# Kernel tuning notes

Hardware: AMD Instinct MI355X
Metric: run time of the kernel (lower is better)

Reference implementation:

```python
import jax, jax.numpy as jnp
import numpy as np

B, N, T, D = 8, 32, 32, 4      # batch, num_atoms, time_steps, dims
K, H, P = 2, 256, 4            # edge_types, decoder_hidden, pred_steps
E = N * (N - 1)                # num directed edges, no self loop
TAU = 0.5                      # gumbel-softmax temperature (hard=False, dropout p=0)


def _onehot_edges():
    idx = np.array([(r, s) for r in range(N) for s in range(N) if r != s], dtype=np.int64)
    eye = np.eye(N, dtype=np.float32)
    return jnp.asarray(eye[idx[:, 0]]), jnp.asarray(eye[idx[:, 1]])  # rel_rec, rel_send [E,N]


def setup_inputs() -> dict:
    key = jax.random.key(0)
    ks = jax.random.split(key, 10)
    rel_rec, rel_send = _onehot_edges()
    u = jax.random.uniform(ks[1], (1, 1, E, K), jnp.float32, 1e-10, 1.0)
    s = 0.05
    return {
        'inputs': jax.random.normal(ks[0], (B, N, T, D), jnp.float32),
        'rel_graph': jax.random.normal(ks[2], (1, 1, E, K), jnp.float32) * (2.0 / (E + K)) ** 0.5,
        'W1': jax.random.normal(ks[3], (K, 2 * D, H), jnp.float32) * s,
        'b1': jnp.zeros((K, H), jnp.float32),
        'W2': jax.random.normal(ks[4], (K, H, H), jnp.float32) * s,
        'b2': jnp.zeros((K, H), jnp.float32),
        'Wo1': jax.random.normal(ks[5], (D + H, H), jnp.float32) * s,
        'bo1': jnp.zeros((H,), jnp.float32),
        'Wo2': jax.random.normal(ks[6], (H, H), jnp.float32) * s,
        'bo2': jnp.zeros((H,), jnp.float32),
        'Wo3': jax.random.normal(ks[7], (H, D), jnp.float32) * s,
        'bo3': jnp.zeros((D,), jnp.float32),
        'rel_rec': rel_rec,
        'rel_send': rel_send,
        'gumbel': -jnp.log(-jnp.log(u)),
    }


def reference(inputs, rel_graph, W1, b1, W2, b2, Wo1, bo1, Wo2, bo2, Wo3, bo3, rel_rec, rel_send, gumbel):
    # gumbel_softmax(rel_graph, tau, hard=False) with fixed gumbel noise
    edges = jax.nn.softmax((rel_graph + gumbel) / TAU, axis=-1)   # [1,1,E,K]
    x = inputs.transpose(0, 2, 1, 3)                              # [B,T,N,D]
    last = x[:, 0::P]                                             # [B,Tp,N,D], Tp = T//P
    preds, hooks = [], []
    for _ in range(P):
        recv = jnp.einsum('en,btnd->bted', rel_rec, last)         # gather receivers
        send = jnp.einsum('en,btnd->bted', rel_send, last)        # gather senders
        pre_msg = jnp.concatenate([send, recv], axis=-1)          # [B,Tp,E,2D]
        all_msgs = jnp.zeros(pre_msg.shape[:3] + (H,), pre_msg.dtype)
        m = None
        for i in range(K):                                        # skip_first=False -> all edge types
            m = jax.nn.relu(pre_msg @ W1[i] + b1[i])              # dropout p=0 -> identity
            m = jax.nn.relu(m @ W2[i] + b2[i])
            m = m * edges[..., i:i + 1]
            all_msgs = all_msgs + m
        hooks.append(m.transpose(1, 0, 2, 3))                     # msg_hook: last type's msg, [Tp,B,E,H]
        agg = jnp.einsum('bteh,en->btnh', all_msgs, rel_rec)      # scatter-sum messages to receivers
        aug = jnp.concatenate([last, agg], axis=-1)               # [B,Tp,N,D+H]
        p = jax.nn.relu(aug @ Wo1 + bo1)
        p = jax.nn.relu(p @ Wo2 + bo2)
        p = p @ Wo3 + bo3
        last = last + p                                           # residual update
        preds.append(last)
    # interleave: output[:, i::P] = preds[i]  ->  time index j*P + i
    out = jnp.stack(preds, axis=2).reshape(B, -1, N, D)           # [B,Tp*P,N,D]
    pred_all = out[:, :T - 1].transpose(0, 2, 1, 3)               # [B,N,T-1,D]
    rel_out = jnp.broadcast_to(rel_graph[:, 0], (B, E, K))
    return pred_all, rel_out, jnp.concatenate(hooks, axis=0)
```

## Files before the change

kernel.cpp:

```cpp
#include <hip/hip_runtime.h>

typedef unsigned short u16;
typedef unsigned int   u32;
typedef unsigned long long u64;
typedef __attribute__((ext_vector_type(8))) short bf16x8;
typedef __attribute__((ext_vector_type(4))) float f32x4;

__device__ __forceinline__ float bf2f(u16 s){ u32 u = ((u32)s)<<16; float f; __builtin_memcpy(&f,&u,4); return f; }
__device__ __forceinline__ u16 f2bf(float f){
  u32 u; __builtin_memcpy(&u,&f,4);
  u32 r = u + 0x7fffu + ((u>>16)&1u);
  return (u16)(r>>16);
}
__device__ __forceinline__ float inV(const void* p, int i, int F){
  return F ? bf2f(((const u16*)p)[i]) : ((const float*)p)[i];
}

__device__ __forceinline__ void detect_bf16(const void* inputs0, int tid, int* flagL){
  if (tid < 64){
    const uint4* dp = (const uint4*)inputs0;
    uint4 v = dp[tid];
    u32 wds[4] = {v.x, v.y, v.z, v.w};
    int sus = 0;
#pragma unroll
    for (int i2=0; i2<4; ++i2){
      u32 wv = wds[i2];
      u32 h0 = wv & 0xffffu, h1 = wv >> 16;
      if (((h0>>7)&0xffu) >= 0xA0u) sus = 1;
      if (((h1>>7)&0xffu) >= 0xA0u) sus = 1;
    }
    u64 bal = __ballot(sus);
    if (tid == 0) *flagL = (bal == 0ull) ? 1 : 0;
  }
}

#define WS_LAST0 0
#define WS_LAST1 32768
#define WS_WF    65536
#define WS_W2P   720896
#define WS_AGG   1245184

#define WF_W1   0
#define WF_B1   4096
#define WF_B2   4608
#define WF_WO1  5120
#define WF_BO1  71680
#define WF_WO2  71936
#define WF_BO2  137472
#define WF_WO3  137728
#define WF_BO3  138752
#define WF_EV   138756

#define PR_WF   138756
#define PR_EV   (PR_WF + 992)
#define PR_L0   (PR_EV + 8192)
#define PR_RO   (PR_L0 + 15872)
#define PR_W2P  (PR_RO + 262144)

__global__ void k_prep(const void* __restrict__ inputs, const void* __restrict__ rel_graph,
                       const void* __restrict__ gumbel,
                       const void* __restrict__ W1, const void* __restrict__ b1,
                       const void* __restrict__ W2, const void* __restrict__ b2,
                       const void* __restrict__ Wo1, const void* __restrict__ bo1,
                       const void* __restrict__ Wo2, const void* __restrict__ bo2,
                       const void* __restrict__ Wo3, const void* __restrict__ bo3,
                       float* __restrict__ wf, u16* __restrict__ w2p,
                       float* __restrict__ last0, float* __restrict__ out)
{
  __shared__ int flagL;
  int tid = threadIdx.x;
  detect_bf16(inputs, tid, &flagL);
  __syncthreads();
  const int F = flagL;
  int i = blockIdx.x*256 + tid;
  if (i < PR_WF){
    const void* src; int off;
    if      (i < 4096)   { src = W1;  off = i; }
    else if (i < 4608)   { src = b1;  off = i-4096; }
    else if (i < 5120)   { src = b2;  off = i-4608; }
    else if (i < 71680)  { src = Wo1; off = i-5120; }
    else if (i < 71936)  { src = bo1; off = i-71680; }
    else if (i < 137472) { src = Wo2; off = i-71936; }
    else if (i < 137728) { src = bo2; off = i-137472; }
    else if (i < 138752) { src = Wo3; off = i-137728; }
    else                 { src = bo3; off = i-138752; }
    wf[i] = inV(src, off, F);
    return;
  }
  if (i < PR_EV){
    int e = i - PR_WF;
    float l0 = (inV(rel_graph,2*e,F)   + inV(gumbel,2*e,F))   * 2.f;
    float l1 = (inV(rel_graph,2*e+1,F) + inV(gumbel,2*e+1,F)) * 2.f;
    float m = fmaxf(l0,l1);
    float e0 = __expf(l0-m), e1 = __expf(l1-m), s = 1.f/(e0+e1);
    wf[WF_EV+2*e]   = e0*s;
    wf[WF_EV+2*e+1] = e1*s;
    return;
  }
  if (i < PR_L0){
    int j = i - PR_EV;
    int d = j&3, n = (j>>2)&31, bt = j>>7, b = bt>>3, tp = bt&7;
    last0[j] = inV(inputs, b*4096 + n*128 + tp*16 + d, F);
    return;
  }
  if (i < PR_RO){
    int j = i - PR_L0;
    out[31744 + j] = inV(rel_graph, j % 1984, F);
    return;
  }
  if (i < PR_W2P){
    int e = i - PR_RO;
    int ei = e & 7, l = (e>>3)&63, q = (e>>9)&7, t = (e>>12)&15,
        part = (e>>16)&1, k = e>>17;
    int kk  = q*32 + (l>>4)*8 + ei;
    int col = t*16 + (l&15);
    float f = inV(W2, k*65536 + kk*256 + col, F);
    u16 h = f2bf(f);
    w2p[e] = part ? f2bf(f - bf2f(h)) : h;
  }
}

__device__ __forceinline__ void fma4(float4& a, float s, float4 w){
  a.x += s*w.x; a.y += s*w.y; a.z += s*w.z; a.w += s*w.w;
}

__global__ __launch_bounds__(256) void k_msg(
    const float* __restrict__ lastIn, const float* __restrict__ wf,
    const u16* __restrict__ w2p, float* __restrict__ agg,
    float* __restrict__ hooks, int pstep)
{
  __shared__ float xj[32][8];
  __shared__ float evL[31][2];
  __shared__ uint4 AhF[16][64];
  __shared__ uint4 AlF[16][64];

  const int tid = threadIdx.x;
  const int n = blockIdx.x & 31, bt = blockIdx.x >> 5;
  const int b = bt>>3, tp = bt&7;
  const int rg = tid & 7, cgi = tid >> 3, c = cgi*8;
  const int lane = tid & 63, wave = tid >> 6;
  const int l15 = lane & 15, lg = lane >> 4;

  if (tid < 32){
    int j = tid;
    float4 sv = make_float4(0.f,0.f,0.f,0.f), rv = sv;
    if (j < 31){
      int s = j + (j >= n);
      sv = *(const float4*)&lastIn[bt*128 + s*4];
      rv = *(const float4*)&lastIn[bt*128 + n*4];
    }
    *(float4*)&xj[j][0] = sv;
    *(float4*)&xj[j][4] = rv;
  } else if (tid < 63){
    int j = tid - 32, e = n*31 + j;
    evL[j][0] = wf[WF_EV + 2*e];
    evL[j][1] = wf[WF_EV + 2*e + 1];
  }
  __syncthreads();

  const int hb = (((pstep*8 + tp)*8 + b)*992 + n*31)*256;
  float aggl[4] = {0.f,0.f,0.f,0.f};

  for (int k=0; k<2; ++k){
    float4 a0[4], a1[4];
    {
      float4 bb0 = *(const float4*)&wf[WF_B1 + k*256 + c];
      float4 bb1 = *(const float4*)&wf[WF_B1 + k*256 + c + 4];
#pragma unroll
      for (int ri=0; ri<4; ++ri){ a0[ri] = bb0; a1[ri] = bb1; }
      const float* W1k = wf + WF_W1 + k*2048;
#pragma unroll
      for (int kd=0; kd<8; ++kd){
        float4 w0 = *(const float4*)&W1k[kd*256 + c];
        float4 w1 = *(const float4*)&W1k[kd*256 + c + 4];
#pragma unroll
        for (int ri=0; ri<4; ++ri){
          float xv = xj[rg + 8*ri][kd];
          fma4(a0[ri], xv, w0); fma4(a1[ri], xv, w1);
        }
      }
    }
    if (k) __syncthreads();
#pragma unroll
    for (int ri=0; ri<4; ++ri){
      int j = rg + 8*ri;
      float v[8] = { fmaxf(a0[ri].x,0.f), fmaxf(a0[ri].y,0.f),
                     fmaxf(a0[ri].z,0.f), fmaxf(a0[ri].w,0.f),
                     fmaxf(a1[ri].x,0.f), fmaxf(a1[ri].y,0.f),
                     fmaxf(a1[ri].z,0.f), fmaxf(a1[ri].w,0.f) };
      u32 hw[4], lw[4];
#pragma unroll
      for (int e2=0; e2<4; ++e2){
        u16 h0 = f2bf(v[2*e2]),   h1 = f2bf(v[2*e2+1]);
        u16 g0 = f2bf(v[2*e2]   - bf2f(h0));
        u16 g1 = f2bf(v[2*e2+1] - bf2f(h1));
        hw[e2] = (u32)h0 | ((u32)h1<<16);
        lw[e2] = (u32)g0 | ((u32)g1<<16);
      }
      int fi   = ((j>>4)<<3) + (cgi>>2);
      int slot = (j&15) + ((cgi&3)<<4);
      AhF[fi][slot] = make_uint4(hw[0],hw[1],hw[2],hw[3]);
      AlF[fi][slot] = make_uint4(lw[0],lw[1],lw[2],lw[3]);
    }
    __syncthreads();

    f32x4 acc[2][4];
#pragma unroll
    for (int nt=0; nt<4; ++nt){
      float bv = wf[WF_B2 + k*256 + wave*64 + nt*16 + l15];
      f32x4 t = {bv,bv,bv,bv};
      acc[0][nt] = t; acc[1][nt] = t;
    }
    const u16* W2pk = w2p + k*131072;
#pragma unroll 2
    for (int q=0; q<8; ++q){
      bf16x8 Ah0 = __builtin_bit_cast(bf16x8, AhF[q][lane]);
      bf16x8 Ah1 = __builtin_bit_cast(bf16x8, AhF[8+q][lane]);
      bf16x8 Al0 = __builtin_bit_cast(bf16x8, AlF[q][lane]);
      bf16x8 Al1 = __builtin_bit_cast(bf16x8, AlF[8+q][lane]);
#pragma unroll
      for (int nt=0; nt<4; ++nt){
        int tt = wave*4 + nt;
        const u16* bp = W2pk + ((tt*8 + q)*64 + lane)*8;
        bf16x8 Bh = __builtin_bit_cast(bf16x8, *(const uint4*)bp);
        bf16x8 Bl = __builtin_bit_cast(bf16x8, *(const uint4*)(bp + 65536));
        acc[0][nt] = __builtin_amdgcn_mfma_f32_16x16x32_bf16(Ah0, Bh, acc[0][nt], 0,0,0);
        acc[1][nt] = __builtin_amdgcn_mfma_f32_16x16x32_bf16(Ah1, Bh, acc[1][nt], 0,0,0);
        acc[0][nt] = __builtin_amdgcn_mfma_f32_16x16x32_bf16(Al0, Bh, acc[0][nt], 0,0,0);
        acc[1][nt] = __builtin_amdgcn_mfma_f32_16x16x32_bf16(Al1, Bh, acc[1][nt], 0,0,0);
        acc[0][nt] = __builtin_amdgcn_mfma_f32_16x16x32_bf16(Ah0, Bl, acc[0][nt], 0,0,0);
        acc[1][nt] = __builtin_amdgcn_mfma_f32_16x16x32_bf16(Ah1, Bl, acc[1][nt], 0,0,0);
      }
    }

#pragma unroll
    for (int rt=0; rt<2; ++rt){
#pragma unroll
      for (int r=0; r<4; ++r){
        int j = rt*16 + lg*4 + r;
        if (j < 31){
          float ev = evL[j][k];
#pragma unroll
          for (int nt=0; nt<4; ++nt){
            float m = fmaxf(acc[rt][nt][r], 0.f) * ev;
            aggl[nt] += m;
            if (k == 1) hooks[hb + j*256 + wave*64 + nt*16 + l15] = m;
          }
        }
      }
    }
  }

#pragma unroll
  for (int nt=0; nt<4; ++nt){
    aggl[nt] += __shfl_xor(aggl[nt], 16);
    aggl[nt] += __shfl_xor(aggl[nt], 32);
  }
  if (lane < 16){
#pragma unroll
    for (int nt=0; nt<4; ++nt)
      agg[blockIdx.x*256 + wave*64 + nt*16 + lane] = aggl[nt];
  }
}

__global__ __launch_bounds__(256) void k_out(
    const float* __restrict__ lastIn, float* __restrict__ lastOut,
    const float* __restrict__ wf, const float* __restrict__ agg,
    float* __restrict__ out0, int pstep)
{
  __shared__ float augT[8][264];
  __shared__ float o1T[8][264];
  __shared__ float o2T[8][264];
  const int tid = threadIdx.x;
  const int r0 = blockIdx.x*8;

#pragma unroll
  for (int rr=0; rr<8; ++rr) augT[rr][4+tid] = agg[(r0+rr)*256 + tid];
  if (tid < 32){
    int rr = tid>>2, d = tid&3, r = r0+rr;
    augT[rr][d] = lastIn[(r>>5)*128 + (r&31)*4 + d];
  }
  __syncthreads();
  {
    float acc[8];
    float bv = wf[WF_BO1 + tid];
#pragma unroll
    for (int rr=0; rr<8; ++rr) acc[rr] = bv;
    for (int i4=0; i4<260; i4+=4){
      float w0 = wf[WF_WO1 + (i4+0)*256 + tid];
      float w1 = wf[WF_WO1 + (i4+1)*256 + tid];
      float w2 = wf[WF_WO1 + (i4+2)*256 + tid];
      float w3 = wf[WF_WO1 + (i4+3)*256 + tid];
#pragma unroll
      for (int rr=0; rr<8; ++rr){
        float4 x = *(const float4*)&augT[rr][i4];
        acc[rr] += x.x*w0 + x.y*w1 + x.z*w2 + x.w*w3;
      }
    }
#pragma unroll
    for (int rr=0; rr<8; ++rr) o1T[rr][tid] = fmaxf(acc[rr], 0.f);
  }
  __syncthreads();
  {
    float acc[8];
    float bv = wf[WF_BO2 + tid];
#pragma unroll
    for (int rr=0; rr<8; ++rr) acc[rr] = bv;
    for (int i4=0; i4<256; i4+=4){
      float w0 = wf[WF_WO2 + (i4+0)*256 + tid];
      float w1 = wf[WF_WO2 + (i4+1)*256 + tid];
      float w2 = wf[WF_WO2 + (i4+2)*256 + tid];
      float w3 = wf[WF_WO2 + (i4+3)*256 + tid];
#pragma unroll
      for (int rr=0; rr<8; ++rr){
        float4 x = *(const float4*)&o1T[rr][i4];
        acc[rr] += x.x*w0 + x.y*w1 + x.z*w2 + x.w*w3;
      }
    }
#pragma unroll
    for (int rr=0; rr<8; ++rr) o2T[rr][tid] = fmaxf(acc[rr], 0.f);
  }
  __syncthreads();
  if (tid < 64){
    int d = tid&3, half = (tid>>2)&1, r = tid>>3;
    float p = 0.f;
    for (int ii=0; ii<128; ++ii){
      int i = half*128 + ii;
      p += o2T[r][i]*wf[WF_WO3 + i*4 + d];
    }
    p += __shfl_xor(p, 4);
    if (!half){
      int row = r0 + r, bt = row>>5, nn = row&31;
      float lv = lastIn[bt*128 + nn*4 + d] + p + wf[WF_BO3 + d];
      lastOut[bt*128 + nn*4 + d] = lv;
      int bb = bt>>3, tp = bt&7, t = tp*4 + pstep;
      if (t < 31) out0[bb*3968 + nn*124 + t*4 + d] = lv;
    }
  }
}

extern "C" void kernel_launch(void* const* d_in, const int* in_sizes, int n_in,
                              void* d_out, int out_size, void* d_ws, size_t ws_size,
                              hipStream_t stream) {
  const void* inputs    = d_in[0];
  const void* rel_graph = d_in[1];
  const void* W1  = d_in[2];
  const void* b1  = d_in[3];
  const void* W2  = d_in[4];
  const void* b2  = d_in[5];
  const void* Wo1 = d_in[6];
  const void* bo1 = d_in[7];
  const void* Wo2 = d_in[8];
  const void* bo2 = d_in[9];
  const void* Wo3 = d_in[10];
  const void* bo3 = d_in[11];
  const void* gumbel = d_in[14];
  float* out = (float*)d_out;
  char* ws = (char*)d_ws;
  float* L0   = (float*)(ws + WS_LAST0);
  float* L1   = (float*)(ws + WS_LAST1);
  float* wf   = (float*)(ws + WS_WF);
  u16*   w2p  = (u16*)  (ws + WS_W2P);
  float* aggp = (float*)(ws + WS_AGG);

  k_prep<<<(PR_W2P + 255)/256, 256, 0, stream>>>(
      inputs, rel_graph, gumbel, W1, b1, W2, b2, Wo1, bo1, Wo2, bo2, Wo3, bo3,
      wf, w2p, L0, out);
  for (int p = 0; p < 4; ++p) {
    const float* lin  = (p & 1) ? L1 : L0;
    float*       lout = (p & 1) ? L0 : L1;
    k_msg<<<2048, 256, 0, stream>>>(lin, wf, w2p, aggp, out + 47616, p);
    k_out<<<256, 256, 0, stream>>>(lin, lout, wf, aggp, out, p);
  }
}
```

Measured before the change: 664.4 us.

## Fuse message and output MLP kernels, switch split-bf16 MFMA to single fp16

Merges the per-step message kernel and the node-output MLP kernel into one kernel, so each block handles two batch-time slices for one receiver node and the aggregated messages stay in shared memory instead of a global round trip. The W2 GEMM goes from a three-pass split-bf16 scheme to one fp16 MFMA pass. Wo1 and Wo2 are pre-transposed and stored as fp16 for vectorized loads. Hook writes are staged through shared memory for coalesced float4 stores. The costs are lower precision in W2 and the output weights, with possible fp16 overflow or accuracy loss, and fewer blocks per launch.

```diff
diff --git a/kernel.cpp b/kernel.cpp
--- a/kernel.cpp
+++ b/kernel.cpp
@@ -3,15 +3,11 @@
 typedef unsigned short u16;
 typedef unsigned int   u32;
 typedef unsigned long long u64;
-typedef __attribute__((ext_vector_type(8))) short bf16x8;
+typedef __attribute__((ext_vector_type(8))) _Float16 f16x8;
 typedef __attribute__((ext_vector_type(4))) float f32x4;
 
 __device__ __forceinline__ float bf2f(u16 s){ u32 u = ((u32)s)<<16; float f; __builtin_memcpy(&f,&u,4); return f; }
-__device__ __forceinline__ u16 f2bf(float f){
-  u32 u; __builtin_memcpy(&u,&f,4);
-  u32 r = u + 0x7fffu + ((u>>16)&1u);
-  return (u16)(r>>16);
-}
+__device__ __forceinline__ u16 f2h(float f){ _Float16 h = (_Float16)f; return __builtin_bit_cast(u16, h); }
 __device__ __forceinline__ float inV(const void* p, int i, int F){
   return F ? bf2f(((const u16*)p)[i]) : ((const float*)p)[i];
 }
@@ -37,25 +33,26 @@
 #define WS_LAST0 0
 #define WS_LAST1 32768
 #define WS_WF    65536
-#define WS_W2P   720896
-#define WS_AGG   1245184
+#define WS_W2P   102400
+#define WS_WO1T  364544
+#define WS_WO2T  499712
 
 #define WF_W1   0
 #define WF_B1   4096
 #define WF_B2   4608
-#define WF_WO1  5120
-#define WF_BO1  71680
-#define WF_WO2  71936
-#define WF_BO2  137472
-#define WF_WO3  137728
-#define WF_BO3  138752
-#define WF_EV   138756
-
-#define PR_WF   138756
-#define PR_EV   (PR_WF + 992)
+#define WF_WO3  5120
+#define WF_BO1  6144
+#define WF_BO2  6400
+#define WF_BO3  6656
+#define WF_EV   6664
+
+#define PR_MISC 6660
+#define PR_EV   (PR_MISC + 992)
 #define PR_L0   (PR_EV + 8192)
 #define PR_RO   (PR_L0 + 15872)
-#define PR_W2P  (PR_RO + 262144)
+#define PR_W2P  (PR_RO + 131072)
+#define PR_WO1T (PR_W2P + 67584)
+#define PR_WO2T (PR_WO1T + 65536)
 
 __global__ void k_prep(const void* __restrict__ inputs, const void* __restrict__ rel_graph,
                        const void* __restrict__ gumbel,
@@ -65,6 +62,7 @@
                        const void* __restrict__ Wo2, const void* __restrict__ bo2,
                        const void* __restrict__ Wo3, const void* __restrict__ bo3,
                        float* __restrict__ wf, u16* __restrict__ w2p,
+                       u16* __restrict__ wo1t, u16* __restrict__ wo2t,
                        float* __restrict__ last0, float* __restrict__ out)
 {
   __shared__ int flagL;
@@ -73,22 +71,20 @@
   __syncthreads();
   const int F = flagL;
   int i = blockIdx.x*256 + tid;
-  if (i < PR_WF){
+  if (i < PR_MISC){
     const void* src; int off;
-    if      (i < 4096)   { src = W1;  off = i; }
-    else if (i < 4608)   { src = b1;  off = i-4096; }
-    else if (i < 5120)   { src = b2;  off = i-4608; }
-    else if (i < 71680)  { src = Wo1; off = i-5120; }
-    else if (i < 71936)  { src = bo1; off = i-71680; }
-    else if (i < 137472) { src = Wo2; off = i-71936; }
-    else if (i < 137728) { src = bo2; off = i-137472; }
-    else if (i < 138752) { src = Wo3; off = i-137728; }
-    else                 { src = bo3; off = i-138752; }
+    if      (i < 4096) { src = W1;  off = i; }
+    else if (i < 4608) { src = b1;  off = i-4096; }
+    else if (i < 5120) { src = b2;  off = i-4608; }
+    else if (i < 6144) { src = Wo3; off = i-5120; }
+    else if (i < 6400) { src = bo1; off = i-6144; }
+    else if (i < 6656) { src = bo2; off = i-6400; }
+    else               { src = bo3; off = i-6656; }
     wf[i] = inV(src, off, F);
     return;
   }
   if (i < PR_EV){
-    int e = i - PR_WF;
+    int e = i - PR_MISC;
     float l0 = (inV(rel_graph,2*e,F)   + inV(gumbel,2*e,F))   * 2.f;
     float l1 = (inV(rel_graph,2*e+1,F) + inV(gumbel,2*e+1,F)) * 2.f;
     float m = fmaxf(l0,l1);
@@ -99,8 +95,8 @@
   }
   if (i < PR_L0){
     int j = i - PR_EV;
-    int d = j&3, n = (j>>2)&31, bt = j>>7, b = bt>>3, tp = bt&7;
-    last0[j] = inV(inputs, b*4096 + n*128 + tp*16 + d, F);
+    int d = j&3, nn = (j>>2)&31, bt = j>>7, b = bt>>3, tp = bt&7;
+    last0[j] = inV(inputs, b*4096 + nn*128 + tp*16 + d, F);
     return;
   }
   if (i < PR_RO){
@@ -110,231 +106,271 @@
   }
   if (i < PR_W2P){
     int e = i - PR_RO;
-    int ei = e & 7, l = (e>>3)&63, q = (e>>9)&7, t = (e>>12)&15,
-        part = (e>>16)&1, k = e>>17;
+    int ei = e & 7, l = (e>>3)&63, q = (e>>9)&7, t = (e>>12)&15, k = e>>16;
     int kk  = q*32 + (l>>4)*8 + ei;
     int col = t*16 + (l&15);
-    float f = inV(W2, k*65536 + kk*256 + col, F);
-    u16 h = f2bf(f);
-    w2p[e] = part ? f2bf(f - bf2f(h)) : h;
+    w2p[e] = f2h(inV(W2, k*65536 + kk*256 + col, F));
+    return;
+  }
+  if (i < PR_WO1T){
+    int e = i - PR_W2P;
+    int c = e / 264, ii = e - c*264;
+    wo1t[e] = (ii < 260) ? f2h(inV(Wo1, ii*256 + c, F)) : (u16)0;
+    return;
+  }
+  if (i < PR_WO2T){
+    int e = i - PR_WO1T;
+    int c = e >> 8, ii = e & 255;
+    wo2t[e] = f2h(inV(Wo2, ii*256 + c, F));
   }
 }
 
 __device__ __forceinline__ void fma4(float4& a, float s, float4 w){
   a.x += s*w.x; a.y += s*w.y; a.z += s*w.z; a.w += s*w.w;
 }
-
-__global__ __launch_bounds__(256) void k_msg(
-    const float* __restrict__ lastIn, const float* __restrict__ wf,
-    const u16* __restrict__ w2p, float* __restrict__ agg,
-    float* __restrict__ hooks, int pstep)
+__device__ __forceinline__ float f4e(const float4& v, int e){
+  switch(e){ case 0: return v.x; case 1: return v.y; case 2: return v.z; default: return v.w; }
+}
+
+__global__ __launch_bounds__(256, 4) void k_fused(
+    const float* __restrict__ lastIn, float* __restrict__ lastOut,
+    const float* __restrict__ wf, const u16* __restrict__ w2p,
+    const u16* __restrict__ wo1t, const u16* __restrict__ wo2t,
+    float* __restrict__ hooks, float* __restrict__ out0, int pstep)
 {
-  __shared__ float xj[32][8];
-  __shared__ float evL[31][2];
-  __shared__ uint4 AhF[16][64];
-  __shared__ uint4 AlF[16][64];
+  __shared__ __align__(16) char smemRaw[35584];
+  float (*xj)[8]  = (float(*)[8])smemRaw;
+  float (*evL)[2] = (float(*)[2])(smemRaw + 2048);
+  uint4* AhF   = (uint4*)(smemRaw + 2304);
+  float* hookT = (float*)(smemRaw + 2304);
+  float* augT  = (float*)(smemRaw + 2304);
+  float* o1T   = (float*)(smemRaw + 2304 + 2112);
+  float* o2T   = (float*)(smemRaw + 2304 + 4224);
 
   const int tid = threadIdx.x;
-  const int n = blockIdx.x & 31, bt = blockIdx.x >> 5;
-  const int b = bt>>3, tp = bt&7;
+  const int n = blockIdx.x & 31, btp = blockIdx.x >> 5;
   const int rg = tid & 7, cgi = tid >> 3, c = cgi*8;
   const int lane = tid & 63, wave = tid >> 6;
   const int l15 = lane & 15, lg = lane >> 4;
 
-  if (tid < 32){
-    int j = tid;
+  if (tid < 64){
+    int e = tid & 31, h = tid >> 5, bt = btp*2 + h;
     float4 sv = make_float4(0.f,0.f,0.f,0.f), rv = sv;
-    if (j < 31){
-      int s = j + (j >= n);
+    if (e < 31){
+      int s = e + (e >= n);
       sv = *(const float4*)&lastIn[bt*128 + s*4];
       rv = *(const float4*)&lastIn[bt*128 + n*4];
     }
-    *(float4*)&xj[j][0] = sv;
-    *(float4*)&xj[j][4] = rv;
-  } else if (tid < 63){
-    int j = tid - 32, e = n*31 + j;
-    evL[j][0] = wf[WF_EV + 2*e];
-    evL[j][1] = wf[WF_EV + 2*e + 1];
+    *(float4*)&xj[tid][0] = sv;
+    *(float4*)&xj[tid][4] = rv;
+  } else if (tid < 95){
+    int e = tid - 64;
+    evL[e][0] = wf[WF_EV + 2*(n*31+e)];
+    evL[e][1] = wf[WF_EV + 2*(n*31+e) + 1];
   }
   __syncthreads();
 
-  const int hb = (((pstep*8 + tp)*8 + b)*992 + n*31)*256;
-  float aggl[4] = {0.f,0.f,0.f,0.f};
+  float agg2[2][4] = {{0.f,0.f,0.f,0.f},{0.f,0.f,0.f,0.f}};
 
   for (int k=0; k<2; ++k){
-    float4 a0[4], a1[4];
+    float4 a[8][2];
     {
       float4 bb0 = *(const float4*)&wf[WF_B1 + k*256 + c];
       float4 bb1 = *(const float4*)&wf[WF_B1 + k*256 + c + 4];
 #pragma unroll
-      for (int ri=0; ri<4; ++ri){ a0[ri] = bb0; a1[ri] = bb1; }
+      for (int ri=0; ri<8; ++ri){ a[ri][0] = bb0; a[ri][1] = bb1; }
       const float* W1k = wf + WF_W1 + k*2048;
 #pragma unroll
-      for (int kd=0; kd<8; ++kd){
-        float4 w0 = *(const float4*)&W1k[kd*256 + c];
-        float4 w1 = *(const float4*)&W1k[kd*256 + c + 4];
+      for (int hf=0; hf<2; ++hf){
+        float4 xr[4][2];
 #pragma unroll
         for (int ri=0; ri<4; ++ri){
-          float xv = xj[rg + 8*ri][kd];
-          fma4(a0[ri], xv, w0); fma4(a1[ri], xv, w1);
+          int j = rg + 8*(hf*4+ri);
+          xr[ri][0] = *(const float4*)&xj[j][0];
+          xr[ri][1] = *(const float4*)&xj[j][4];
         }
-      }
-    }
-    if (k) __syncthreads();
-#pragma unroll
-    for (int ri=0; ri<4; ++ri){
-      int j = rg + 8*ri;
-      float v[8] = { fmaxf(a0[ri].x,0.f), fmaxf(a0[ri].y,0.f),
-                     fmaxf(a0[ri].z,0.f), fmaxf(a0[ri].w,0.f),
-                     fmaxf(a1[ri].x,0.f), fmaxf(a1[ri].y,0.f),
-                     fmaxf(a1[ri].z,0.f), fmaxf(a1[ri].w,0.f) };
-      u32 hw[4], lw[4];
-#pragma unroll
-      for (int e2=0; e2<4; ++e2){
-        u16 h0 = f2bf(v[2*e2]),   h1 = f2bf(v[2*e2+1]);
-        u16 g0 = f2bf(v[2*e2]   - bf2f(h0));
-        u16 g1 = f2bf(v[2*e2+1] - bf2f(h1));
-        hw[e2] = (u32)h0 | ((u32)h1<<16);
-        lw[e2] = (u32)g0 | ((u32)g1<<16);
-      }
-      int fi   = ((j>>4)<<3) + (cgi>>2);
-      int slot = (j&15) + ((cgi&3)<<4);
-      AhF[fi][slot] = make_uint4(hw[0],hw[1],hw[2],hw[3]);
-      AlF[fi][slot] = make_uint4(lw[0],lw[1],lw[2],lw[3]);
-    }
-    __syncthreads();
-
-    f32x4 acc[2][4];
-#pragma unroll
-    for (int nt=0; nt<4; ++nt){
-      float bv = wf[WF_B2 + k*256 + wave*64 + nt*16 + l15];
-      f32x4 t = {bv,bv,bv,bv};
-      acc[0][nt] = t; acc[1][nt] = t;
-    }
-    const u16* W2pk = w2p + k*131072;
-#pragma unroll 2
-    for (int q=0; q<8; ++q){
-      bf16x8 Ah0 = __builtin_bit_cast(bf16x8, AhF[q][lane]);
-      bf16x8 Ah1 = __builtin_bit_cast(bf16x8, AhF[8+q][lane]);
-      bf16x8 Al0 = __builtin_bit_cast(bf16x8, AlF[q][lane]);
-      bf16x8 Al1 = __builtin_bit_cast(bf16x8, AlF[8+q][lane]);
-#pragma unroll
-      for (int nt=0; nt<4; ++nt){
-        int tt = wave*4 + nt;
-        const u16* bp = W2pk + ((tt*8 + q)*64 + lane)*8;
-        bf16x8 Bh = __builtin_bit_cast(bf16x8, *(const uint4*)bp);
-        bf16x8 Bl = __builtin_bit_cast(bf16x8, *(const uint4*)(bp + 65536));
-        acc[0][nt] = __builtin_amdgcn_mfma_f32_16x16x32_bf16(Ah0, Bh, acc[0][nt], 0,0,0);
-        acc[1][nt] = __builtin_amdgcn_mfma_f32_16x16x32_bf16(Ah1, Bh, acc[1][nt], 0,0,0);
-        acc[0][nt] = __builtin_amdgcn_mfma_f32_16x16x32_bf16(Al0, Bh, acc[0][nt], 0,0,0);
-        acc[1][nt] = __builtin_amdgcn_mfma_f32_16x16x32_bf16(Al1, Bh, acc[1][nt], 0,0,0);
-        acc[0][nt] = __builtin_amdgcn_mfma_f32_16x16x32_bf16(Ah0, Bl, acc[0][nt], 0,0,0);
-        acc[1][nt] = __builtin_amdgcn_mfma_f32_16x16x32_bf16(Ah1, Bl, acc[1][nt], 0,0,0);
-      }
-    }
-
-#pragma unroll
-    for (int rt=0; rt<2; ++rt){
-#pragma unroll
-      for (int r=0; r<4; ++r){
-        int j = rt*16 + lg*4 + r;
-        if (j < 31){
-          float ev = evL[j][k];
-#pragma unroll
-          for (int nt=0; nt<4; ++nt){
-            float m = fmaxf(acc[rt][nt][r], 0.f) * ev;
-            aggl[nt] += m;
-            if (k == 1) hooks[hb + j*256 + wave*64 + nt*16 + l15] = m;
+#pragma unroll
+        for (int kd=0; kd<8; ++kd){
+          float4 w0 = *(const float4*)&W1k[kd*256 + c];
+          float4 w1 = *(const float4*)&W1k[kd*256 + c + 4];
+#pragma unroll
+          for (int ri=0; ri<4; ++ri){
+            float xv = f4e(xr[ri][kd>>2], kd&3);
+            fma4(a[hf*4+ri][0], xv, w0); fma4(a[hf*4+ri][1], xv, w1);
           }
         }
       }
     }
-  }
-
-#pragma unroll
-  for (int nt=0; nt<4; ++nt){
-    aggl[nt] += __shfl_xor(aggl[nt], 16);
-    aggl[nt] += __shfl_xor(aggl[nt], 32);
-  }
-  if (lane < 16){
-#pragma unroll
-    for (int nt=0; nt<4; ++nt)
-      agg[blockIdx.x*256 + wave*64 + nt*16 + lane] = aggl[nt];
-  }
-}
-
-__global__ __launch_bounds__(256) void k_out(
-    const float* __restrict__ lastIn, float* __restrict__ lastOut,
-    const float* __restrict__ wf, const float* __restrict__ agg,
-    float* __restrict__ out0, int pstep)
-{
-  __shared__ float augT[8][264];
-  __shared__ float o1T[8][264];
-  __shared__ float o2T[8][264];
-  const int tid = threadIdx.x;
-  const int r0 = blockIdx.x*8;
-
-#pragma unroll
-  for (int rr=0; rr<8; ++rr) augT[rr][4+tid] = agg[(r0+rr)*256 + tid];
-  if (tid < 32){
-    int rr = tid>>2, d = tid&3, r = r0+rr;
-    augT[rr][d] = lastIn[(r>>5)*128 + (r&31)*4 + d];
+    if (k) __syncthreads();
+#pragma unroll
+    for (int ri=0; ri<8; ++ri){
+      int j = rg + 8*ri;
+      f16x8 hv;
+#pragma unroll
+      for (int e2=0; e2<8; ++e2)
+        hv[e2] = (_Float16)fmaxf(f4e(a[ri][e2>>2], e2&3), 0.f);
+      int fi   = ((j>>4)<<3) + (cgi>>2);
+      int slot = (j&15) + ((cgi&3)<<4);
+      AhF[fi*64 + slot] = __builtin_bit_cast(uint4, hv);
+    }
+    __syncthreads();
+
+    f32x4 acc[4][4];
+#pragma unroll
+    for (int nt=0; nt<4; ++nt){
+      float bv = wf[WF_B2 + k*256 + (wave<<6) + (nt<<4) + l15];
+      f32x4 bi = {bv,bv,bv,bv};
+#pragma unroll
+      for (int rt=0; rt<4; ++rt) acc[rt][nt] = bi;
+    }
+    const u16* Bbase = w2p + ((k*16 + (wave<<2))*8)*512 + (lane<<3);
+#pragma unroll
+    for (int q=0; q<8; ++q){
+      uint4 Au[4];
+#pragma unroll
+      for (int rt=0; rt<4; ++rt) Au[rt] = AhF[(rt*8+q)*64 + lane];
+#pragma unroll
+      for (int nt=0; nt<4; ++nt){
+        f16x8 Bf = __builtin_bit_cast(f16x8, *(const uint4*)(Bbase + nt*4096 + q*512));
+#pragma unroll
+        for (int rt=0; rt<4; ++rt)
+          acc[rt][nt] = __builtin_amdgcn_mfma_f32_16x16x32_f16(
+              __builtin_bit_cast(f16x8, Au[rt]), Bf, acc[rt][nt], 0,0,0);
+      }
+    }
+
+    if (k == 0){
+#pragma unroll
+      for (int rt=0; rt<4; ++rt){
+#pragma unroll
+        for (int r=0; r<4; ++r){
+          int lr = ((rt&1)<<4) + (lg<<2) + r;
+          if (lr < 31){
+            float ev = evL[lr][0];
+#pragma unroll
+            for (int nt=0; nt<4; ++nt)
+              agg2[rt>>1][nt] += fmaxf(acc[rt][nt][r], 0.f)*ev;
+          }
+        }
+      }
+    } else {
+      __syncthreads();
+#pragma unroll
+      for (int h=0; h<2; ++h){
+#pragma unroll
+        for (int rt2=0; rt2<2; ++rt2){
+          int rt = h*2 + rt2;
+#pragma unroll
+          for (int r=0; r<4; ++r){
+            int lr = (rt2<<4) + (lg<<2) + r;
+            if (lr < 31){
+              float ev = evL[lr][1];
+#pragma unroll
+              for (int nt=0; nt<4; ++nt){
+                float m = fmaxf(acc[rt][nt][r], 0.f)*ev;
+                agg2[h][nt] += m;
+                hookT[lr*260 + (wave<<6) + (nt<<4) + l15] = m;
+              }
+            }
+          }
+        }
+        __syncthreads();
+        {
+          int bt = btp*2 + h, bb = bt>>3, tp = bt&7;
+          int hbh = (((pstep*8 + tp)*8 + bb)*992 + n*31)*256;
+#pragma unroll
+          for (int it=0; it<8; ++it){
+            int row = wave + (it<<2);
+            if (row < 31){
+              float4 v = *(const float4*)&hookT[row*260 + (lane<<2)];
+              *(float4*)&hooks[hbh + row*256 + (lane<<2)] = v;
+            }
+          }
+        }
+        __syncthreads();
+      }
+    }
+  }
+
+#pragma unroll
+  for (int h=0; h<2; ++h)
+#pragma unroll
+    for (int nt=0; nt<4; ++nt){
+      float v = agg2[h][nt];
+      v += __shfl_xor(v, 16);
+      v += __shfl_xor(v, 32);
+      agg2[h][nt] = v;
+    }
+  if (lg == 0){
+#pragma unroll
+    for (int h=0; h<2; ++h)
+#pragma unroll
+      for (int nt=0; nt<4; ++nt)
+        augT[h*264 + 4 + (wave<<6) + (nt<<4) + l15] = agg2[h][nt];
+  }
+  if (tid < 8){
+    int h = tid>>2, d = tid&3;
+    augT[h*264 + d] = lastIn[(btp*2+h)*128 + n*4 + d];
+  } else if (tid < 16){
+    int h = (tid-8)>>2, d = (tid-8)&3;
+    augT[h*264 + 260 + d] = 0.f;
+  }
+  __syncthreads();
+
+  {
+    const u16* wc = wo1t + tid*264;
+    float s0 = wf[WF_BO1 + tid], s1 = s0;
+    for (int i=0; i<264; i+=8){
+      f16x8 hw = __builtin_bit_cast(f16x8, *(const uint4*)(wc + i));
+      float4 xa0 = *(const float4*)&augT[i];
+      float4 xa1 = *(const float4*)&augT[i+4];
+      float4 xb0 = *(const float4*)&augT[264+i];
+      float4 xb1 = *(const float4*)&augT[264+i+4];
+      float w0=(float)hw[0], w1=(float)hw[1], w2=(float)hw[2], w3=(float)hw[3];
+      float w4=(float)hw[4], w5=(float)hw[5], w6=(float)hw[6], w7=(float)hw[7];
+      s0 += xa0.x*w0 + xa0.y*w1 + xa0.z*w2 + xa0.w*w3
+          + xa1.x*w4 + xa1.y*w5 + xa1.z*w6 + xa1.w*w7;
+      s1 += xb0.x*w0 + xb0.y*w1 + xb0.z*w2 + xb0.w*w3
+          + xb1.x*w4 + xb1.y*w5 + xb1.z*w6 + xb1.w*w7;
+    }
+    o1T[tid] = fmaxf(s0, 0.f); o1T[264 + tid] = fmaxf(s1, 0.f);
   }
   __syncthreads();
   {
-    float acc[8];
-    float bv = wf[WF_BO1 + tid];
-#pragma unroll
-    for (int rr=0; rr<8; ++rr) acc[rr] = bv;
-    for (int i4=0; i4<260; i4+=4){
-      float w0 = wf[WF_WO1 + (i4+0)*256 + tid];
-      float w1 = wf[WF_WO1 + (i4+1)*256 + tid];
-      float w2 = wf[WF_WO1 + (i4+2)*256 + tid];
-      float w3 = wf[WF_WO1 + (i4+3)*256 + tid];
-#pragma unroll
-      for (int rr=0; rr<8; ++rr){
-        float4 x = *(const float4*)&augT[rr][i4];
-        acc[rr] += x.x*w0 + x.y*w1 + x.z*w2 + x.w*w3;
-      }
-    }
-#pragma unroll
-    for (int rr=0; rr<8; ++rr) o1T[rr][tid] = fmaxf(acc[rr], 0.f);
+    const u16* wc = wo2t + tid*256;
+    float s0 = wf[WF_BO2 + tid], s1 = s0;
+    for (int i=0; i<256; i+=8){
+      f16x8 hw = __builtin_bit_cast(f16x8, *(const uint4*)(wc + i));
+      float4 xa0 = *(const float4*)&o1T[i];
+      float4 xa1 = *(const float4*)&o1T[i+4];
+      float4 xb0 = *(const float4*)&o1T[264+i];
+      float4 xb1 = *(const float4*)&o1T[264+i+4];
+      float w0=(float)hw[0], w1=(float)hw[1], w2=(float)hw[2], w3=(float)hw[3];
+      float w4=(float)hw[4], w5=(float)hw[5], w6=(float)hw[6], w7=(float)hw[7];
+      s0 += xa0.x*w0 + xa0.y*w1 + xa0.z*w2 + xa0.w*w3
+          + xa1.x*w4 + xa1.y*w5 + xa1.z*w6 + xa1.w*w7;
+      s1 += xb0.x*w0 + xb0.y*w1 + xb0.z*w2 + xb0.w*w3
+          + xb1.x*w4 + xb1.y*w5 + xb1.z*w6 + xb1.w*w7;
+    }
+    o2T[tid] = fmaxf(s0, 0.f); o2T[264 + tid] = fmaxf(s1, 0.f);
   }
   __syncthreads();
-  {
-    float acc[8];
-    float bv = wf[WF_BO2 + tid];
-#pragma unroll
-    for (int rr=0; rr<8; ++rr) acc[rr] = bv;
-    for (int i4=0; i4<256; i4+=4){
-      float w0 = wf[WF_WO2 + (i4+0)*256 + tid];
-      float w1 = wf[WF_WO2 + (i4+1)*256 + tid];
-      float w2 = wf[WF_WO2 + (i4+2)*256 + tid];
-      float w3 = wf[WF_WO2 + (i4+3)*256 + tid];
-#pragma unroll
-      for (int rr=0; rr<8; ++rr){
-        float4 x = *(const float4*)&o1T[rr][i4];
-        acc[rr] += x.x*w0 + x.y*w1 + x.z*w2 + x.w*w3;
-      }
-    }
-#pragma unroll
-    for (int rr=0; rr<8; ++rr) o2T[rr][tid] = fmaxf(acc[rr], 0.f);
-  }
-  __syncthreads();
-  if (tid < 64){
-    int d = tid&3, half = (tid>>2)&1, r = tid>>3;
+  if (tid < 128){
+    int h = tid>>6, d = tid&3, ch = (tid>>2)&15;
     float p = 0.f;
-    for (int ii=0; ii<128; ++ii){
-      int i = half*128 + ii;
-      p += o2T[r][i]*wf[WF_WO3 + i*4 + d];
-    }
-    p += __shfl_xor(p, 4);
-    if (!half){
-      int row = r0 + r, bt = row>>5, nn = row&31;
-      float lv = lastIn[bt*128 + nn*4 + d] + p + wf[WF_BO3 + d];
-      lastOut[bt*128 + nn*4 + d] = lv;
+#pragma unroll
+    for (int ii=0; ii<16; ++ii){
+      int i = ch*16 + ii;
+      p += o2T[h*264 + i]*wf[WF_WO3 + i*4 + d];
+    }
+    p += __shfl_xor(p, 4); p += __shfl_xor(p, 8);
+    p += __shfl_xor(p, 16); p += __shfl_xor(p, 32);
+    if (ch == 0){
+      int bt = btp*2 + h;
+      float lv = lastIn[bt*128 + n*4 + d] + p + wf[WF_BO3 + d];
+      lastOut[bt*128 + n*4 + d] = lv;
       int bb = bt>>3, tp = bt&7, t = tp*4 + pstep;
-      if (t < 31) out0[bb*3968 + nn*124 + t*4 + d] = lv;
+      if (t < 31) out0[bb*3968 + n*124 + t*4 + d] = lv;
     }
   }
 }
@@ -361,15 +397,16 @@
   float* L1   = (float*)(ws + WS_LAST1);
   float* wf   = (float*)(ws + WS_WF);
   u16*   w2p  = (u16*)  (ws + WS_W2P);
-  float* aggp = (float*)(ws + WS_AGG);
-
-  k_prep<<<(PR_W2P + 255)/256, 256, 0, stream>>>(
+  u16*   wo1t = (u16*)  (ws + WS_WO1T);
+  u16*   wo2t = (u16*)  (ws + WS_WO2T);
+
+  k_prep<<<(PR_WO2T + 255)/256, 256, 0, stream>>>(
       inputs, rel_graph, gumbel, W1, b1, W2, b2, Wo1, bo1, Wo2, bo2, Wo3, bo3,
-      wf, w2p, L0, out);
+      wf, w2p, wo1t, wo2t, L0, out);
   for (int p = 0; p < 4; ++p) {
     const float* lin  = (p & 1) ? L1 : L0;
     float*       lout = (p & 1) ? L0 : L1;
-    k_msg<<<2048, 256, 0, stream>>>(lin, wf, w2p, aggp, out + 47616, p);
-    k_out<<<256, 256, 0, stream>>>(lin, lout, wf, aggp, out, p);
-  }
-}
+    k_fused<<<1024, 256, 0, stream>>>(lin, lout, wf, w2p, wo1t, wo2t,
+                                      out + 47616, out, p);
+  }
+}
```

New measurement: 667.6 us. About the same (+0.5%).
